# Kernel optimization log

Hardware: AMD Instinct MI355X
Metric: run time of the kernel (lower is better)

## Reference

```python
import jax, jax.numpy as jnp
import numpy as np

EPS = 1e-8


def _lstm_cell(xx, h, c, Wih, Whh, bih, bhh):
    g = xx @ Wih.T + bih + h @ Whh.T + bhh
    i, f, gg, o = jnp.split(g, 4, axis=-1)
    i = jax.nn.sigmoid(i); f = jax.nn.sigmoid(f); o = jax.nn.sigmoid(o)
    c2 = f * c + i * jnp.tanh(gg)
    return o * jnp.tanh(c2), c2


def _layernorm(t):
    mu = t.mean(-1, keepdims=True)
    var = t.var(-1, keepdims=True)
    return (t - mu) / jnp.sqrt(var + 1e-5)


def _dnc_forward(x, memory0, Wy, WE, Wr, lstm_params):
    bs, T, xd = x.shape
    N, W = memory0.shape[1], memory0.shape[2]
    R = Wr.shape[0] // W
    hdim = lstm_params[0][1].shape[2]
    L = len(lstm_params)

    def step(carry, x_t):
        M, lrw, u, lww, lrv, h, c = carry
        # BatchNorm1d (training-mode batch stats, affine=identity)
        bn = (x_t - x_t.mean(0)) / jnp.sqrt(x_t.var(0) + 1e-5)
        layer_in = jnp.concatenate([bn, lrv.reshape(bs, W * R)], axis=1)
        # bidirectional multi-layer LSTM, single timestep
        hs, cs = [], []
        for l in range(L):
            Wih, Whh, bih, bhh = lstm_params[l]
            hf, cf = _lstm_cell(layer_in, h[2 * l], c[2 * l], Wih[0], Whh[0], bih[0], bhh[0])
            hb, cb = _lstm_cell(layer_in, h[2 * l + 1], c[2 * l + 1], Wih[1], Whh[1], bih[1], bhh[1])
            layer_in = jnp.concatenate([hf, hb], axis=1)
            hs += [hf, hb]; cs += [cf, cb]
        h_new = jnp.stack(hs); c_new = jnp.stack(cs)  # (2L, bs, h)
        flat = jnp.transpose(h_new, (1, 0, 2)).reshape(bs, 2 * L * hdim)
        vt = flat @ Wy
        iv = _layernorm(flat @ WE)
        # interface parsing (E_t = W*R + 3W + 3R + 3)
        i0 = W * R
        rkeys = iv[:, :i0].reshape(bs, W, R)
        rbeta = 1.0 - jax.nn.log_sigmoid(iv[:, i0:i0 + R]); i0 += R
        wkey = iv[:, i0:i0 + W]; i0 += W
        wbeta = 1.0 - jax.nn.log_sigmoid(iv[:, i0:i0 + 1]); i0 += 1
        erase = jax.nn.sigmoid(iv[:, i0:i0 + W]); i0 += W
        wvec = iv[:, i0:i0 + W]; i0 += W
        fgates = jax.nn.sigmoid(iv[:, i0:i0 + R]); i0 += R
        ag = jax.nn.sigmoid(iv[:, i0:i0 + 1]); i0 += 1
        wg = jax.nn.sigmoid(iv[:, i0:i0 + 1]); i0 += 1
        # read_modes: softmax over a singleton dim -> all ones (content-only read)
        # memory retention and usage
        retention = jnp.prod(1.0 - fgates[:, None, :] * lrw, axis=2)  # (bs, N)
        u_new = (u + lww - u * lww) * retention
        # allocation weighting (sort ascending usage, exclusive cumprod)
        idx = jnp.argsort(u_new, axis=1)
        su = jnp.take_along_axis(u_new, idx, axis=1)
        cp = jnp.cumprod(su, axis=1)
        cp = jnp.concatenate([jnp.ones((bs, 1), su.dtype), cp[:, :-1]], axis=1)
        a_sorted = (1.0 - su) * cp
        alloc = jnp.take_along_axis(a_sorted, jnp.argsort(idx, axis=1), axis=1)
        # write weighting: content + allocation
        Mn = M / (jnp.linalg.norm(M, axis=2, keepdims=True) + EPS)
        kn = wkey / (jnp.linalg.norm(wkey, axis=1, keepdims=True) + EPS)
        cw = jax.nn.softmax(wbeta * jnp.einsum('bnw,bw->bn', Mn, kn), axis=1)
        ww = wg * (ag * alloc + (1.0 - ag) * cw)  # (bs, N)
        # write to memory
        M_new = M * (1.0 - ww[:, :, None] * erase[:, None, :]) + ww[:, :, None] * wvec[:, None, :]
        # content read weightings against updated memory
        Mn2 = M_new / (jnp.linalg.norm(M_new, axis=2, keepdims=True) + EPS)
        rkn = rkeys / (jnp.linalg.norm(rkeys, axis=1, keepdims=True) + EPS)
        sim = jnp.einsum('bnw,bwr->bnr', Mn2, rkn)
        rw = jax.nn.softmax(rbeta[:, None, :] * sim, axis=1)  # (bs, N, R)
        rv = jnp.einsum('bnw,bnr->bwr', M_new, rw)            # (bs, W, R)
        yt = vt + rv.reshape(bs, W * R) @ Wr
        return (M_new, rw, u_new, ww, rv, h_new, c_new), yt

    z = lambda *s: jnp.zeros(s, x.dtype)
    init = (memory0, z(bs, N, R), z(bs, N), z(bs, N), z(bs, W, R),
            z(2 * L, bs, hdim), z(2 * L, bs, hdim))
    _, yts = jax.lax.scan(step, init, jnp.transpose(x, (1, 0, 2)))
    return jnp.max(yts, axis=0)  # max over timesteps, (bs, v_t)


def setup_inputs() -> dict:
    key = jax.random.key(0)
    ks = jax.random.split(key, 16)
    bs, T, xd = 32, 32, 128
    hdim, L, v_t, W, R, N = 512, 2, 2048, 64, 4, 1024
    E_t = W * R + 3 * W + 3 * R + 3  # 463
    u = lambda k, shape, s: jax.random.uniform(k, shape, jnp.float32, -s, s)
    in0, in1 = xd + R * W, 2 * hdim
    sh = 1.0 / np.sqrt(hdim)
    inp = {
        'x': jax.random.normal(ks[0], (bs, T, xd), jnp.float32),
        'memory0': u(ks[1], (bs, N, W), 1.0 / np.sqrt(W)),
        'Wy': u(ks[2], (2 * L * hdim, v_t), 1.0 / np.sqrt(v_t)),
        'WE': u(ks[3], (2 * L * hdim, E_t), 1.0 / np.sqrt(E_t)),
        'Wr': u(ks[4], (W * R, v_t), 1.0 / np.sqrt(v_t)),
        'Wih0': u(ks[5], (2, 4 * hdim, in0), sh),
        'Whh0': u(ks[6], (2, 4 * hdim, hdim), sh),
        'bih0': u(ks[7], (2, 4 * hdim), sh),
        'bhh0': u(ks[8], (2, 4 * hdim), sh),
        'Wih1': u(ks[9], (2, 4 * hdim, in1), sh),
        'Whh1': u(ks[10], (2, 4 * hdim, hdim), sh),
        'bih1': u(ks[11], (2, 4 * hdim), sh),
        'bhh1': u(ks[12], (2, 4 * hdim), sh),
    }
    return inp


def reference(x, memory0, Wy, WE, Wr, Wih0, Whh0, bih0, bhh0, Wih1, Whh1, bih1, bhh1):
    lstm_params = [(Wih0, Whh0, bih0, bhh0), (Wih1, Whh1, bih1, bhh1)]
    return _dnc_forward(x, memory0, Wy, WE, Wr, lstm_params)
```

## Files before the change

### kernel.cpp

```cpp
#include <hip/hip_runtime.h>
#include <math.h>

#define BSZ 32
#define TT  32
#define XD  128
#define HD  512
#define VT  2048
#define ET  463
#define GKS 8
#define VKS 16

__device__ __forceinline__ float sigf(float x){ return 1.f/(1.f+expf(-x)); }
__device__ __forceinline__ float logsigf(float x){
    return (x >= 0.f) ? -log1pf(expf(-x)) : x - log1pf(expf(x));
}

__device__ __forceinline__ float bsum(float v, float* red, int tid){
    #pragma unroll
    for (int off = 32; off > 0; off >>= 1) v += __shfl_xor(v, off);
    if ((tid & 63) == 0) red[tid >> 6] = v;
    __syncthreads();
    if (tid == 0){
        float s = red[0];
        #pragma unroll
        for (int i = 1; i < 16; ++i) s += red[i];
        red[16] = s;
    }
    __syncthreads();
    float r = red[16];
    __syncthreads();
    return r;
}
__device__ __forceinline__ float bmax(float v, float* red, int tid){
    #pragma unroll
    for (int off = 32; off > 0; off >>= 1) v = fmaxf(v, __shfl_xor(v, off));
    if ((tid & 63) == 0) red[tid >> 6] = v;
    __syncthreads();
    if (tid == 0){
        float s = red[0];
        #pragma unroll
        for (int i = 1; i < 16; ++i) s = fmaxf(s, red[i]);
        red[16] = s;
    }
    __syncthreads();
    float r = red[16];
    __syncthreads();
    return r;
}

__global__ void dnc_bnx(const float* __restrict__ x, float* __restrict__ bnx){
    int t = blockIdx.x, k = threadIdx.x;
    float vals[BSZ];
    float s = 0.f;
    #pragma unroll
    for (int b = 0; b < BSZ; ++b){ vals[b] = x[(b*TT + t)*XD + k]; s += vals[b]; }
    float mean = s * (1.f/BSZ);
    float ss = 0.f;
    #pragma unroll
    for (int b = 0; b < BSZ; ++b){ float d = vals[b]-mean; ss += d*d; }
    float inv = 1.f / sqrtf(ss*(1.f/BSZ) + 1e-5f);
    #pragma unroll
    for (int b = 0; b < BSZ; ++b) bnx[((size_t)t*BSZ + b)*XD + k] = (vals[b]-mean)*inv;
}

__device__ __forceinline__ void lstm_gemm_body(
    const float* __restrict__ srcA, int KA,
    const float* __restrict__ srcB, int KB,
    const float* __restrict__ hbase,
    const float* __restrict__ Wih, const float* __restrict__ Whh,
    float* __restrict__ gpart, int jc, int d, int ks, int tid,
    float* itile, float* wtile)
{
    const int jg = tid & 31, bg = tid >> 5;
    const int jbase = jc*128;
    const int j0 = jbase + jg*4;
    const int jg4 = jg*4;
    const int b0 = bg*4;
    const int K1 = KA + KB;
    const int cA = KA >> 6;
    const int cin = K1 >> 6;
    const int nct = cin + 8;
    const int per = (nct + GKS - 1) / GKS;
    int c0 = ks*per; int c1 = min(nct, c0+per);
    float acc[4][4] = {{0}};
    for (int c = c0; c < c1; ++c){
        const float* src; int stride, kb, wcol; const float* Wb; int Kw;
        if (c < cA){ src = srcA; stride = KA; kb = c*64; wcol = c*64;
                     Wb = Wih + (size_t)d*2048*K1; Kw = K1; }
        else if (c < cin){ src = srcB; stride = KB; kb = (c-cA)*64; wcol = c*64;
                           Wb = Wih + (size_t)d*2048*K1; Kw = K1; }
        else { src = hbase + d*(BSZ*HD); stride = HD; kb = (c-cin)*64; wcol = kb;
               Wb = Whh + (size_t)d*2048*512; Kw = 512; }
        #pragma unroll
        for (int i = 0; i < 8; ++i){
            int idx = i*256 + tid; int kk = idx & 63, b = idx >> 6;
            itile[kk*36 + b] = src[b*stride + kb + kk];
        }
        #pragma unroll
        for (int i = 0; i < 8; ++i){
            int fi = i*256 + tid;
            int j  = fi & 127;
            int kq = fi >> 7;
            float4 w4 = *(const float4*)&Wb[(size_t)(jbase + j)*Kw + wcol + kq*4];
            wtile[(kq*4+0)*132 + j] = w4.x;
            wtile[(kq*4+1)*132 + j] = w4.y;
            wtile[(kq*4+2)*132 + j] = w4.z;
            wtile[(kq*4+3)*132 + j] = w4.w;
        }
        __syncthreads();
        #pragma unroll 8
        for (int kk = 0; kk < 64; ++kk){
            float4 a = *(const float4*)&itile[kk*36 + b0];
            float4 w = *(const float4*)&wtile[kk*132 + jg4];
            acc[0][0] += w.x*a.x; acc[0][1] += w.x*a.y; acc[0][2] += w.x*a.z; acc[0][3] += w.x*a.w;
            acc[1][0] += w.y*a.x; acc[1][1] += w.y*a.y; acc[1][2] += w.y*a.z; acc[1][3] += w.y*a.w;
            acc[2][0] += w.z*a.x; acc[2][1] += w.z*a.y; acc[2][2] += w.z*a.z; acc[2][3] += w.z*a.w;
            acc[3][0] += w.w*a.x; acc[3][1] += w.w*a.y; acc[3][2] += w.w*a.z; acc[3][3] += w.w*a.w;
        }
        __syncthreads();
    }
    #pragma unroll
    for (int jj = 0; jj < 4; ++jj){
        #pragma unroll
        for (int bb = 0; bb < 4; ++bb)
            gpart[((size_t)(d*GKS + ks)*BSZ + (b0+bb))*2048 + (j0+jj)] = acc[jj][bb];
    }
}

__device__ __forceinline__ void yfin_body(
    const float* __restrict__ lrv, const float* __restrict__ Wr,
    const float* __restrict__ vtp, float* __restrict__ out, int t,
    int mi, int bgi, int tid, float* lt)
{
    const int mg = tid & 31, bgl = tid >> 5;
    const int m0 = mi*128 + mg*4;
    const int b  = bgi*8 + bgl;
    #pragma unroll
    for (int i = 0; i < 8; ++i)
        lt[tid*9 + i] = lrv[((size_t)(bgi*8 + i))*256 + tid];
    __syncthreads();
    float4 acc = make_float4(0.f,0.f,0.f,0.f);
    for (int kk = 0; kk < 256; ++kk){
        float av = lt[kk*9 + bgl];
        float4 wv = *(const float4*)&Wr[(size_t)kk*VT + m0];
        acc.x += av*wv.x; acc.y += av*wv.y; acc.z += av*wv.z; acc.w += av*wv.w;
    }
    #pragma unroll
    for (int sp = 0; sp < VKS; ++sp){
        float4 vp = *(const float4*)&vtp[((size_t)sp*BSZ + b)*VT + m0];
        acc.x += vp.x; acc.y += vp.y; acc.z += vp.z; acc.w += vp.w;
    }
    float4* op = (float4*)&out[(size_t)b*VT + m0];
    if (t == 0){ *op = acc; }
    else {
        float4 cur = *op;
        cur.x = fmaxf(cur.x, acc.x); cur.y = fmaxf(cur.y, acc.y);
        cur.z = fmaxf(cur.z, acc.z); cur.w = fmaxf(cur.w, acc.w);
        *op = cur;
    }
}

__global__ __launch_bounds__(256) void dnc_gemm0_yfin(
    const float* __restrict__ srcA,
    const float* __restrict__ lrv, const float* __restrict__ hbase,
    const float* __restrict__ Wih, const float* __restrict__ Whh,
    float* __restrict__ gpart,
    const float* __restrict__ Wr, const float* __restrict__ vtp,
    float* __restrict__ out, int tprev)
{
    __shared__ __align__(16) float itile[64*36];
    __shared__ __align__(16) float wtile[64*132];
    const int bid = blockIdx.x, tid = threadIdx.x;
    if (bid < 256){
        lstm_gemm_body(srcA, XD, lrv, 256, hbase, Wih, Whh, gpart,
                       bid & 15, (bid >> 4) & 1, bid >> 5, tid, itile, wtile);
    } else {
        if (tprev < 0) return;
        int yb = bid - 256;
        yfin_body(lrv, Wr, vtp, out, tprev, yb & 15, yb >> 4, tid, itile);
    }
}

__global__ __launch_bounds__(256) void dnc_lstm_gemm(
    const float* __restrict__ srcA, int KA,
    const float* __restrict__ srcB, int KB,
    const float* __restrict__ hbase,
    const float* __restrict__ Wih, const float* __restrict__ Whh,
    float* __restrict__ gpart)
{
    __shared__ __align__(16) float itile[64*36];
    __shared__ __align__(16) float wtile[64*132];
    lstm_gemm_body(srcA, KA, srcB, KB, hbase, Wih, Whh, gpart,
                   blockIdx.x, blockIdx.y, blockIdx.z, threadIdx.x, itile, wtile);
}

__global__ void dnc_yfin(const float* __restrict__ lrv, const float* __restrict__ Wr,
                         const float* __restrict__ vtp, float* __restrict__ out, int t){
    __shared__ float lt[256*9];
    yfin_body(lrv, Wr, vtp, out, t, blockIdx.x, blockIdx.y, threadIdx.x, lt);
}

__global__ void dnc_gates(const float* __restrict__ gpart,
                          const float* __restrict__ bih, const float* __restrict__ bhh,
                          float* __restrict__ cstate, float* __restrict__ hwrite,
                          float* __restrict__ flat, float* __restrict__ lout, int l){
    int idx = blockIdx.x*256 + threadIdx.x;
    int u = idx & 511, b = (idx >> 9) & 31, d = idx >> 14;
    int cell = 2*l + d;
    float g[4];
    #pragma unroll
    for (int xg = 0; xg < 4; ++xg){
        int j = xg*512 + u;
        float s = bih[d*2048 + j] + bhh[d*2048 + j];
        #pragma unroll
        for (int ks = 0; ks < GKS; ++ks)
            s += gpart[((size_t)(d*GKS + ks)*BSZ + b)*2048 + j];
        g[xg] = s;
    }
    float ig = sigf(g[0]), fg = sigf(g[1]), og = sigf(g[3]);
    float gg = tanhf(g[2]);
    int ci = (cell*BSZ + b)*HD + u;
    float c2 = fg*cstate[ci] + ig*gg;
    cstate[ci] = c2;
    float h = og*tanhf(c2);
    hwrite[ci] = h;
    flat[b*2048 + cell*HD + u] = h;
    if (lout) lout[b*1024 + d*HD + u] = h;
}

__global__ void dnc_gemv2(const float* __restrict__ fin, const float* __restrict__ Wy,
                          const float* __restrict__ WE,
                          float* __restrict__ vtp, float* __restrict__ ep){
    const int bx = blockIdx.x, ksi = blockIdx.y;
    const int tid = threadIdx.x;
    const int lane = tid & 63, bg = tid >> 6;
    const int b0 = bg*8;
    const int k0 = ksi*128;
    __shared__ __align__(16) float tile[128*36];
    #pragma unroll
    for (int i = 0; i < 16; ++i){
        int idx = i*256 + tid; int kk = idx & 127, b = idx >> 7;
        tile[kk*36 + b] = fin[b*2048 + k0 + kk];
    }
    __syncthreads();

    if (bx < 8){
        const int m = bx*256 + lane*4;
        float acc[8][4] = {{0}};
        #pragma unroll 4
        for (int kk = 0; kk < 128; ++kk){
            float4 w  = *(const float4*)&Wy[(size_t)(k0+kk)*VT + m];
            float4 a0 = *(const float4*)&tile[kk*36 + b0];
            float4 a1 = *(const float4*)&tile[kk*36 + b0 + 4];
            acc[0][0]+=a0.x*w.x; acc[0][1]+=a0.x*w.y; acc[0][2]+=a0.x*w.z; acc[0][3]+=a0.x*w.w;
            acc[1][0]+=a0.y*w.x; acc[1][1]+=a0.y*w.y; acc[1][2]+=a0.y*w.z; acc[1][3]+=a0.y*w.w;
            acc[2][0]+=a0.z*w.x; acc[2][1]+=a0.z*w.y; acc[2][2]+=a0.z*w.z; acc[2][3]+=a0.z*w.w;
            acc[3][0]+=a0.w*w.x; acc[3][1]+=a0.w*w.y; acc[3][2]+=a0.w*w.z; acc[3][3]+=a0.w*w.w;
            acc[4][0]+=a1.x*w.x; acc[4][1]+=a1.x*w.y; acc[4][2]+=a1.x*w.z; acc[4][3]+=a1.x*w.w;
            acc[5][0]+=a1.y*w.x; acc[5][1]+=a1.y*w.y; acc[5][2]+=a1.y*w.z; acc[5][3]+=a1.y*w.w;
            acc[6][0]+=a1.z*w.x; acc[6][1]+=a1.z*w.y; acc[6][2]+=a1.z*w.z; acc[6][3]+=a1.z*w.w;
            acc[7][0]+=a1.w*w.x; acc[7][1]+=a1.w*w.y; acc[7][2]+=a1.w*w.z; acc[7][3]+=a1.w*w.w;
        }
        #pragma unroll
        for (int bb = 0; bb < 8; ++bb){
            float4 st = make_float4(acc[bb][0], acc[bb][1], acc[bb][2], acc[bb][3]);
            *(float4*)&vtp[((size_t)ksi*BSZ + b0+bb)*VT + m] = st;
        }
    } else {
        const int mb = bx - 8;
        const int m0 = mb*128 + lane, m1 = m0 + 64;
        bool v0 = m0 < ET, v1 = m1 < ET;
        float acc[16] = {0};
        #pragma unroll 2
        for (int kk = 0; kk < 128; ++kk){
            float4 pq = *(const float4*)&tile[kk*36 + b0];
            float4 qq = *(const float4*)&tile[kk*36 + b0 + 4];
            const float* wr = WE + (size_t)(k0+kk)*ET;
            float w0 = v0 ? wr[m0] : 0.f;
            float w1 = v1 ? wr[m1] : 0.f;
            acc[0]+=pq.x*w0; acc[1]+=pq.y*w0; acc[2]+=pq.z*w0; acc[3]+=pq.w*w0;
            acc[4]+=qq.x*w0; acc[5]+=qq.y*w0; acc[6]+=qq.z*w0; acc[7]+=qq.w*w0;
            acc[8]+=pq.x*w1; acc[9]+=pq.y*w1; acc[10]+=pq.z*w1; acc[11]+=pq.w*w1;
            acc[12]+=qq.x*w1; acc[13]+=qq.y*w1; acc[14]+=qq.z*w1; acc[15]+=qq.w*w1;
        }
        if (v0){
            #pragma unroll
            for (int bb = 0; bb < 8; ++bb)
                ep[((size_t)ksi*BSZ + b0+bb)*ET + m0] = acc[bb];
        }
        if (v1){
            #pragma unroll
            for (int bb = 0; bb < 8; ++bb)
                ep[((size_t)ksi*BSZ + b0+bb)*ET + m1] = acc[8+bb];
        }
    }
}

__global__ __launch_bounds__(1024) void dnc_presort_cw(
    const float* __restrict__ ep, const float* __restrict__ lrw,
    const float* __restrict__ lww, float* __restrict__ ubuf,
    float* __restrict__ iv, float* __restrict__ allocw,
    const float* __restrict__ M, float* __restrict__ scw)
{
    const int bid = blockIdx.x, tid = threadIdx.x;
    const int lane = tid & 63, wid = tid >> 6;
    __shared__ float red[32];
    __shared__ float ivS[464];
    __shared__ unsigned long long keysS[1024];
    __shared__ float wtot[16], wpref[16];

    if (bid < 32){
        const int b = bid;
        float myv = 0.f;
        if (tid < ET){
            #pragma unroll
            for (int s = 0; s < VKS; ++s) myv += ep[((size_t)s*BSZ + b)*ET + tid];
        }
        float mean = bsum(myv, red, tid) * (1.f/ET);
        float dd = (tid < ET) ? (myv - mean) : 0.f;
        float var = bsum(dd*dd, red, tid) * (1.f/ET);
        float rinv = 1.f / sqrtf(var + 1e-5f);
        float ivv = (myv - mean)*rinv;
        if (tid < ET){ ivS[tid] = ivv; iv[b*ET + tid] = ivv; }
        __syncthreads();

        const int n = tid;
        float4 lw4 = *(const float4*)&lrw[((size_t)b*1024 + n)*4];
        float f0 = sigf(ivS[453]), f1 = sigf(ivS[454]), f2 = sigf(ivS[455]), f3 = sigf(ivS[456]);
        float ret = (1.f-f0*lw4.x)*(1.f-f1*lw4.y)*(1.f-f2*lw4.z)*(1.f-f3*lw4.w);
        float uo = ubuf[b*1024+n], lwo = lww[b*1024+n];
        float un = (uo + lwo - uo*lwo)*ret;
        ubuf[b*1024+n] = un;

        unsigned long long key = ((unsigned long long)__float_as_uint(un) << 32) | (unsigned)tid;
        for (int k = 2; k <= 1024; k <<= 1){
            int j = k >> 1;
            for (; j >= 64; j >>= 1){
                keysS[tid] = key; __syncthreads();
                unsigned long long other = keysS[tid ^ j];
                bool up = ((tid & k) == 0);
                bool takeMin = (((tid & j) == 0) == up);
                key = takeMin ? (key < other ? key : other) : (key > other ? key : other);
                __syncthreads();
            }
            for (; j >= 1; j >>= 1){
                unsigned long long other = __shfl_xor(key, j);
                bool up = ((tid & k) == 0);
                bool takeMin = (((tid & j) == 0) == up);
                key = takeMin ? (key < other ? key : other) : (key > other ? key : other);
            }
        }
        float su = __uint_as_float((unsigned)(key >> 32));
        int idxv = (int)(key & 0xffffffffu);

        float p = su;
        #pragma unroll
        for (int o = 1; o < 64; o <<= 1){ float q = __shfl_up(p, o); if (lane >= o) p *= q; }
        if (lane == 63) wtot[wid] = p;
        __syncthreads();
        if (tid == 0){
            float r = 1.f;
            #pragma unroll
            for (int i = 0; i < 16; ++i){ wpref[i] = r; r *= wtot[i]; }
        }
        __syncthreads();
        float excl = __shfl_up(p, 1); if (lane == 0) excl = 1.f;
        float cpx = excl * wpref[wid];
        allocw[b*1024 + idxv] = (1.f - su)*cpx;
    } else {
        const int b = bid - 32;
        float myv = 0.f;
        if (tid < ET){
            #pragma unroll
            for (int s = 0; s < VKS; ++s) myv += ep[((size_t)s*BSZ + b)*ET + tid];
        }
        float mean = bsum(myv, red, tid) * (1.f/ET);
        float dd = (tid < ET) ? (myv - mean) : 0.f;
        float var = bsum(dd*dd, red, tid) * (1.f/ET);
        float rinv = 1.f / sqrtf(var + 1e-5f);
        float ivv = (myv - mean)*rinv;
        if (tid >= 260 && tid < 324) ivS[tid - 260] = ivv;
        if (tid == 324) ivS[64] = 1.f - logsigf(ivv);
        __syncthreads();
        float ksq = 0.f;
        #pragma unroll
        for (int w = 0; w < 64; ++w) ksq += ivS[w]*ivS[w];
        float kden = sqrtf(ksq) + 1e-8f;
        float wb = ivS[64];
        const float* Mrow = M + ((size_t)b*1024 + tid)*64;
        float dot = 0.f, msq = 0.f;
        #pragma unroll
        for (int w = 0; w < 64; w += 4){
            float4 mv = *(const float4*)(Mrow + w);
            dot += mv.x*ivS[w] + mv.y*ivS[w+1] + mv.z*ivS[w+2] + mv.w*ivS[w+3];
            msq += mv.x*mv.x + mv.y*mv.y + mv.z*mv.z + mv.w*mv.w;
        }
        scw[b*1024 + tid] = wb*dot/((sqrtf(msq) + 1e-8f)*kden);
    }
}

__global__ __launch_bounds__(1024) void dnc_memup_rv(
    float* __restrict__ M, const float* __restrict__ scw,
    const float* __restrict__ allocw, const float* __restrict__ iv,
    float* __restrict__ lww, float* __restrict__ lrw, float* __restrict__ lrv)
{
    const int b = blockIdx.x, tid = threadIdx.x;
    const int lane = tid & 63, wid = tid >> 6;
    __shared__ float red[32];
    __shared__ float aux[400];
    __shared__ float pS[4096];
    __shared__ float rvS[4096];
    const int n = tid;

    float s = scw[b*1024 + n];
    float mx = bmax(s, red, tid);
    float tot = bsum(expf(s - mx), red, tid);
    float cwv = expf(s - mx)/tot;
    float ag = sigf(iv[b*ET + 457]), wg = sigf(iv[b*ET + 458]);
    float wwv = wg*(ag*allocw[b*1024 + n] + (1.f-ag)*cwv);
    lww[b*1024 + n] = wwv;

    if (tid < 64){ aux[tid] = sigf(iv[b*ET + 325 + tid]); aux[64+tid] = iv[b*ET + 389 + tid]; }
    if (tid >= 64 && tid < 320) aux[64 + tid] = iv[b*ET + (tid - 64)];
    if (tid >= 320 && tid < 324) aux[72 + tid] = 1.f - logsigf(iv[b*ET + 256 + (tid - 320)]);
    __syncthreads();
    if (tid < 4){
        float ss = 0.f;
        #pragma unroll
        for (int w = 0; w < 64; ++w){ float v = aux[128 + w*4 + tid]; ss += v*v; }
        aux[384 + tid] = sqrtf(ss) + 1e-8f;
    }
    __syncthreads();
    if (tid < 256) aux[128 + tid] = aux[128 + tid] / aux[384 + (tid & 3)];
    __syncthreads();

    float* Mrow = M + ((size_t)b*1024 + n)*64;
    float dr0=0.f, dr1=0.f, dr2=0.f, dr3=0.f, msq2=0.f;
    #pragma unroll
    for (int w = 0; w < 64; w += 4){
        float4 mv = *(const float4*)(Mrow + w);
        mv.x = mv.x*(1.f - wwv*aux[w+0]) + wwv*aux[64+w+0];
        mv.y = mv.y*(1.f - wwv*aux[w+1]) + wwv*aux[64+w+1];
        mv.z = mv.z*(1.f - wwv*aux[w+2]) + wwv*aux[64+w+2];
        mv.w = mv.w*(1.f - wwv*aux[w+3]) + wwv*aux[64+w+3];
        *(float4*)(Mrow + w) = mv;
        msq2 += mv.x*mv.x + mv.y*mv.y + mv.z*mv.z + mv.w*mv.w;
        dr0 += mv.x*aux[128+(w+0)*4+0] + mv.y*aux[128+(w+1)*4+0] + mv.z*aux[128+(w+2)*4+0] + mv.w*aux[128+(w+3)*4+0];
        dr1 += mv.x*aux[128+(w+0)*4+1] + mv.y*aux[128+(w+1)*4+1] + mv.z*aux[128+(w+2)*4+1] + mv.w*aux[128+(w+3)*4+1];
        dr2 += mv.x*aux[128+(w+0)*4+2] + mv.y*aux[128+(w+1)*4+2] + mv.z*aux[128+(w+2)*4+2] + mv.w*aux[128+(w+3)*4+2];
        dr3 += mv.x*aux[128+(w+0)*4+3] + mv.y*aux[128+(w+1)*4+3] + mv.z*aux[128+(w+2)*4+3] + mv.w*aux[128+(w+3)*4+3];
    }
    float den = sqrtf(msq2) + 1e-8f;
    pS[0*1024 + n] = aux[392]*dr0/den;
    pS[1*1024 + n] = aux[393]*dr1/den;
    pS[2*1024 + n] = aux[394]*dr2/den;
    pS[3*1024 + n] = aux[395]*dr3/den;
    __syncthreads();

    const int r_ = tid >> 8, i4 = (tid & 255)*4;
    float v0 = pS[r_*1024 + i4+0], v1 = pS[r_*1024 + i4+1];
    float v2 = pS[r_*1024 + i4+2], v3 = pS[r_*1024 + i4+3];
    float lm = fmaxf(fmaxf(v0,v1), fmaxf(v2,v3));
    #pragma unroll
    for (int off = 32; off > 0; off >>= 1) lm = fmaxf(lm, __shfl_xor(lm, off));
    if (lane == 0) red[wid] = lm;
    __syncthreads();
    if (tid < 4) red[16+tid] = fmaxf(fmaxf(red[4*tid],red[4*tid+1]), fmaxf(red[4*tid+2],red[4*tid+3]));
    __syncthreads();
    float mxr = red[16 + r_];
    float lsum = expf(v0-mxr) + expf(v1-mxr) + expf(v2-mxr) + expf(v3-mxr);
    #pragma unroll
    for (int off = 32; off > 0; off >>= 1) lsum += __shfl_xor(lsum, off);
    if (lane == 0) red[wid] = lsum;
    __syncthreads();
    if (tid < 4) red[20+tid] = red[4*tid]+red[4*tid+1]+red[4*tid+2]+red[4*tid+3];
    __syncthreads();
    float totr = red[20 + r_];
    {
        lrw[((size_t)(b*1024 + i4+0))*4 + r_] = expf(v0-mxr)/totr;
        lrw[((size_t)(b*1024 + i4+1))*4 + r_] = expf(v1-mxr)/totr;
        lrw[((size_t)(b*1024 + i4+2))*4 + r_] = expf(v2-mxr)/totr;
        lrw[((size_t)(b*1024 + i4+3))*4 + r_] = expf(v3-mxr)/totr;
    }
    __syncthreads();

    {
        const int w = tid & 63, g = tid >> 6;
        const float* Mb = M + (size_t)b*65536;
        const float* rwb = lrw + (size_t)b*4096;
        float a0=0.f, a1=0.f, a2=0.f, a3=0.f;
        #pragma unroll 4
        for (int i = 0; i < 64; ++i){
            int n2 = g*64 + i;
            float m = Mb[(size_t)n2*64 + w];
            float4 rw4 = *(const float4*)&rwb[n2*4];
            a0 += m*rw4.x; a1 += m*rw4.y; a2 += m*rw4.z; a3 += m*rw4.w;
        }
        rvS[(0*16 + g)*64 + w] = a0;
        rvS[(1*16 + g)*64 + w] = a1;
        rvS[(2*16 + g)*64 + w] = a2;
        rvS[(3*16 + g)*64 + w] = a3;
    }
    __syncthreads();
    if (tid < 256){
        int w2 = tid >> 2, r2 = tid & 3;
        float ssum = 0.f;
        #pragma unroll
        for (int g = 0; g < 16; ++g) ssum += rvS[(r2*16 + g)*64 + w2];
        lrv[b*256 + tid] = ssum;
    }
}

extern "C" void kernel_launch(void* const* d_in, const int* in_sizes, int n_in,
                              void* d_out, int out_size, void* d_ws, size_t ws_size,
                              hipStream_t stream){
    const float* x      = (const float*)d_in[0];
    const float* mem0   = (const float*)d_in[1];
    const float* Wy     = (const float*)d_in[2];
    const float* WE     = (const float*)d_in[3];
    const float* Wr     = (const float*)d_in[4];
    const float* Wih0   = (const float*)d_in[5];
    const float* Whh0   = (const float*)d_in[6];
    const float* bih0   = (const float*)d_in[7];
    const float* bhh0   = (const float*)d_in[8];
    const float* Wih1   = (const float*)d_in[9];
    const float* Whh1   = (const float*)d_in[10];
    const float* bih1   = (const float*)d_in[11];
    const float* bhh1   = (const float*)d_in[12];
    float* out = (float*)d_out;

    float* p = (float*)d_ws;
    float* M       = p; p += (size_t)BSZ*1024*64;
    float* hstate0 = p; p += 4*BSZ*HD;
    float* hstate1 = p; p += 4*BSZ*HD;
    float* cstate  = p; p += 4*BSZ*HD;
    float* ubuf    = p; p += BSZ*1024;
    float* lww     = p; p += BSZ*1024;
    float* lrw     = p; p += BSZ*1024*4;
    float* lrv     = p; p += BSZ*256;
    float* bnx     = p; p += (size_t)TT*BSZ*XD;
    float* lin1    = p; p += BSZ*1024;
    float* gpart   = p; p += (size_t)2*GKS*BSZ*2048;
    float* flat    = p; p += BSZ*2048;
    float* vtp     = p; p += (size_t)VKS*BSZ*VT;
    float* ep      = p; p += (size_t)VKS*BSZ*ET;
    float* iv      = p; p += BSZ*ET;
    float* allocw  = p; p += BSZ*1024;
    float* scw     = p; p += BSZ*1024;

    (void)hipMemcpyAsync(M, mem0, (size_t)BSZ*1024*64*sizeof(float), hipMemcpyDeviceToDevice, stream);
    size_t zfloats = (size_t)(4*BSZ*HD)*3 + BSZ*1024*2 + BSZ*1024*4 + BSZ*256;
    (void)hipMemsetAsync(hstate0, 0, zfloats*sizeof(float), stream);

    dnc_bnx<<<TT, 128, 0, stream>>>(x, bnx);

    for (int t = 0; t < TT; ++t){
        const float* hr = (t & 1) ? hstate1 : hstate0;
        float*       hw = (t & 1) ? hstate0 : hstate1;
        dnc_gemm0_yfin<<<320, 256, 0, stream>>>(bnx + (size_t)t*BSZ*XD,
            lrv, hr, Wih0, Whh0, gpart, Wr, vtp, out, t - 1);
        dnc_gates<<<128, 256, 0, stream>>>(gpart, bih0, bhh0, cstate, hw, flat, lin1, 0);
        dnc_lstm_gemm<<<dim3(16,2,GKS), 256, 0, stream>>>(lin1, 1024,
            nullptr, 0, hr + 2*BSZ*HD, Wih1, Whh1, gpart);
        dnc_gates<<<128, 256, 0, stream>>>(gpart, bih1, bhh1, cstate, hw, flat, nullptr, 1);
        dnc_gemv2<<<dim3(12,VKS), 256, 0, stream>>>(flat, Wy, WE, vtp, ep);
        dnc_presort_cw<<<64, 1024, 0, stream>>>(ep, lrw, lww, ubuf, iv, allocw, M, scw);
        dnc_memup_rv<<<32, 1024, 0, stream>>>(M, scw, allocw, iv, lww, lrw, lrv);
    }
    dnc_yfin<<<dim3(16,4), 256, 0, stream>>>(lrv, Wr, vtp, out, TT - 1);
}
```

Measured before the change: 3.919 ms.

## Move Wy GEMV into presort kernel and prefetch weights in registers

The fused output/interface GEMV is split. The WE (interface) part stays as its own small kernel on the critical path. The Wy (output vector) part is moved into extra blocks of the presort/content-weight kernel, so it overlaps with the memory-addressing work instead of delaying it. Both GEMV loops now software-prefetch the next 8 weight rows into registers. The cost is higher register pressure and a larger presort launch, whose 1024-thread Wy blocks use more shared memory.

Result: slower. 8.823 ms (+125.1%).

```diff
diff --git a/kernel.cpp b/kernel.cpp
--- a/kernel.cpp
+++ b/kernel.cpp
@@ -228,13 +228,13 @@
     if (lout) lout[b*1024 + d*HD + u] = h;
 }
 
-__global__ void dnc_gemv2(const float* __restrict__ fin, const float* __restrict__ Wy,
-                          const float* __restrict__ WE,
-                          float* __restrict__ vtp, float* __restrict__ ep){
-    const int bx = blockIdx.x, ksi = blockIdx.y;
+__global__ void dnc_gemv_we(const float* __restrict__ fin, const float* __restrict__ WE,
+                            float* __restrict__ ep){
+    const int mb = blockIdx.x, ksi = blockIdx.y;
     const int tid = threadIdx.x;
     const int lane = tid & 63, bg = tid >> 6;
     const int b0 = bg*8;
+    const int m0 = mb*128 + lane, m1 = m0 + 64;
     const int k0 = ksi*128;
     __shared__ __align__(16) float tile[128*36];
     #pragma unroll
@@ -243,56 +243,43 @@
         tile[kk*36 + b] = fin[b*2048 + k0 + kk];
     }
     __syncthreads();
-
-    if (bx < 8){
-        const int m = bx*256 + lane*4;
-        float acc[8][4] = {{0}};
-        #pragma unroll 4
-        for (int kk = 0; kk < 128; ++kk){
-            float4 w  = *(const float4*)&Wy[(size_t)(k0+kk)*VT + m];
-            float4 a0 = *(const float4*)&tile[kk*36 + b0];
-            float4 a1 = *(const float4*)&tile[kk*36 + b0 + 4];
-            acc[0][0]+=a0.x*w.x; acc[0][1]+=a0.x*w.y; acc[0][2]+=a0.x*w.z; acc[0][3]+=a0.x*w.w;
-            acc[1][0]+=a0.y*w.x; acc[1][1]+=a0.y*w.y; acc[1][2]+=a0.y*w.z; acc[1][3]+=a0.y*w.w;
-            acc[2][0]+=a0.z*w.x; acc[2][1]+=a0.z*w.y; acc[2][2]+=a0.z*w.z; acc[2][3]+=a0.z*w.w;
-            acc[3][0]+=a0.w*w.x; acc[3][1]+=a0.w*w.y; acc[3][2]+=a0.w*w.z; acc[3][3]+=a0.w*w.w;
-            acc[4][0]+=a1.x*w.x; acc[4][1]+=a1.x*w.y; acc[4][2]+=a1.x*w.z; acc[4][3]+=a1.x*w.w;
-            acc[5][0]+=a1.y*w.x; acc[5][1]+=a1.y*w.y; acc[5][2]+=a1.y*w.z; acc[5][3]+=a1.y*w.w;
-            acc[6][0]+=a1.z*w.x; acc[6][1]+=a1.z*w.y; acc[6][2]+=a1.z*w.z; acc[6][3]+=a1.z*w.w;
-            acc[7][0]+=a1.w*w.x; acc[7][1]+=a1.w*w.y; acc[7][2]+=a1.w*w.z; acc[7][3]+=a1.w*w.w;
-        }
-        #pragma unroll
-        for (int bb = 0; bb < 8; ++bb){
-            float4 st = make_float4(acc[bb][0], acc[bb][1], acc[bb][2], acc[bb][3]);
-            *(float4*)&vtp[((size_t)ksi*BSZ + b0+bb)*VT + m] = st;
-        }
-    } else {
-        const int mb = bx - 8;
-        const int m0 = mb*128 + lane, m1 = m0 + 64;
-        bool v0 = m0 < ET, v1 = m1 < ET;
-        float acc[16] = {0};
-        #pragma unroll 2
-        for (int kk = 0; kk < 128; ++kk){
+    bool v0 = m0 < ET, v1 = m1 < ET;
+    float w0r[8], w1r[8];
+    #pragma unroll
+    for (int i = 0; i < 8; ++i){
+        const float* wr = WE + (size_t)(k0+i)*ET;
+        w0r[i] = v0 ? wr[m0] : 0.f;
+        w1r[i] = v1 ? wr[m1] : 0.f;
+    }
+    float acc[16] = {0};
+    for (int kb = 0; kb < 128; kb += 8){
+        #pragma unroll
+        for (int i = 0; i < 8; ++i){
+            int kk = kb + i;
+            float w0 = w0r[i], w1 = w1r[i];
+            int kn = kk + 8;
+            if (kn < 128){
+                const float* wr = WE + (size_t)(k0+kn)*ET;
+                w0r[i] = v0 ? wr[m0] : 0.f;
+                w1r[i] = v1 ? wr[m1] : 0.f;
+            }
             float4 pq = *(const float4*)&tile[kk*36 + b0];
             float4 qq = *(const float4*)&tile[kk*36 + b0 + 4];
-            const float* wr = WE + (size_t)(k0+kk)*ET;
-            float w0 = v0 ? wr[m0] : 0.f;
-            float w1 = v1 ? wr[m1] : 0.f;
             acc[0]+=pq.x*w0; acc[1]+=pq.y*w0; acc[2]+=pq.z*w0; acc[3]+=pq.w*w0;
             acc[4]+=qq.x*w0; acc[5]+=qq.y*w0; acc[6]+=qq.z*w0; acc[7]+=qq.w*w0;
             acc[8]+=pq.x*w1; acc[9]+=pq.y*w1; acc[10]+=pq.z*w1; acc[11]+=pq.w*w1;
             acc[12]+=qq.x*w1; acc[13]+=qq.y*w1; acc[14]+=qq.z*w1; acc[15]+=qq.w*w1;
         }
-        if (v0){
-            #pragma unroll
-            for (int bb = 0; bb < 8; ++bb)
-                ep[((size_t)ksi*BSZ + b0+bb)*ET + m0] = acc[bb];
-        }
-        if (v1){
-            #pragma unroll
-            for (int bb = 0; bb < 8; ++bb)
-                ep[((size_t)ksi*BSZ + b0+bb)*ET + m1] = acc[8+bb];
-        }
+    }
+    if (v0){
+        #pragma unroll
+        for (int bb = 0; bb < 8; ++bb)
+            ep[((size_t)ksi*BSZ + b0+bb)*ET + m0] = acc[bb];
+    }
+    if (v1){
+        #pragma unroll
+        for (int bb = 0; bb < 8; ++bb)
+            ep[((size_t)ksi*BSZ + b0+bb)*ET + m1] = acc[8+bb];
     }
 }
 
@@ -300,7 +287,9 @@
     const float* __restrict__ ep, const float* __restrict__ lrw,
     const float* __restrict__ lww, float* __restrict__ ubuf,
     float* __restrict__ iv, float* __restrict__ allocw,
-    const float* __restrict__ M, float* __restrict__ scw)
+    const float* __restrict__ M, float* __restrict__ scw,
+    const float* __restrict__ fin, const float* __restrict__ Wy,
+    float* __restrict__ vtp)
 {
     const int bid = blockIdx.x, tid = threadIdx.x;
     const int lane = tid & 63, wid = tid >> 6;
@@ -308,6 +297,7 @@
     __shared__ float ivS[464];
     __shared__ unsigned long long keysS[1024];
     __shared__ float wtot[16], wpref[16];
+    __shared__ __align__(16) float tile[128*36];
 
     if (bid < 32){
         const int b = bid;
@@ -367,7 +357,7 @@
         float excl = __shfl_up(p, 1); if (lane == 0) excl = 1.f;
         float cpx = excl * wpref[wid];
         allocw[b*1024 + idxv] = (1.f - su)*cpx;
-    } else {
+    } else if (bid < 64){
         const int b = bid - 32;
         float myv = 0.f;
         if (tid < ET){
@@ -396,6 +386,48 @@
             msq += mv.x*mv.x + mv.y*mv.y + mv.z*mv.z + mv.w*mv.w;
         }
         scw[b*1024 + tid] = wb*dot/((sqrtf(msq) + 1e-8f)*kden);
+    } else {
+        const int yb = bid - 64;
+        const int ksi = yb >> 1, half = yb & 1;
+        const int k0 = ksi*128;
+        #pragma unroll
+        for (int i = 0; i < 4; ++i){
+            int idx = i*1024 + tid; int kk = idx & 127, b = idx >> 7;
+            tile[kk*36 + b] = fin[b*2048 + k0 + kk];
+        }
+        __syncthreads();
+        const int sub = tid >> 8, stid = tid & 255;
+        const int slane = stid & 63, sbg = stid >> 6;
+        const int b0 = sbg*8;
+        const int m = (half*4 + sub)*256 + slane*4;
+        float4 wreg[8];
+        #pragma unroll
+        for (int i = 0; i < 8; ++i) wreg[i] = *(const float4*)&Wy[(size_t)(k0+i)*VT + m];
+        float acc[8][4] = {{0}};
+        for (int kb = 0; kb < 128; kb += 8){
+            #pragma unroll
+            for (int i = 0; i < 8; ++i){
+                const int kk = kb + i;
+                float4 w = wreg[i];
+                int kn = kk + 8;
+                if (kn < 128) wreg[i] = *(const float4*)&Wy[(size_t)(k0+kn)*VT + m];
+                float4 a0 = *(const float4*)&tile[kk*36 + b0];
+                float4 a1 = *(const float4*)&tile[kk*36 + b0 + 4];
+                acc[0][0]+=a0.x*w.x; acc[0][1]+=a0.x*w.y; acc[0][2]+=a0.x*w.z; acc[0][3]+=a0.x*w.w;
+                acc[1][0]+=a0.y*w.x; acc[1][1]+=a0.y*w.y; acc[1][2]+=a0.y*w.z; acc[1][3]+=a0.y*w.w;
+                acc[2][0]+=a0.z*w.x; acc[2][1]+=a0.z*w.y; acc[2][2]+=a0.z*w.z; acc[2][3]+=a0.z*w.w;
+                acc[3][0]+=a0.w*w.x; acc[3][1]+=a0.w*w.y; acc[3][2]+=a0.w*w.z; acc[3][3]+=a0.w*w.w;
+                acc[4][0]+=a1.x*w.x; acc[4][1]+=a1.x*w.y; acc[4][2]+=a1.x*w.z; acc[4][3]+=a1.x*w.w;
+                acc[5][0]+=a1.y*w.x; acc[5][1]+=a1.y*w.y; acc[5][2]+=a1.y*w.z; acc[5][3]+=a1.y*w.w;
+                acc[6][0]+=a1.z*w.x; acc[6][1]+=a1.z*w.y; acc[6][2]+=a1.z*w.z; acc[6][3]+=a1.z*w.w;
+                acc[7][0]+=a1.w*w.x; acc[7][1]+=a1.w*w.y; acc[7][2]+=a1.w*w.z; acc[7][3]+=a1.w*w.w;
+            }
+        }
+        #pragma unroll
+        for (int bb = 0; bb < 8; ++bb){
+            float4 st = make_float4(acc[bb][0], acc[bb][1], acc[bb][2], acc[bb][3]);
+            *(float4*)&vtp[((size_t)ksi*BSZ + b0+bb)*VT + m] = st;
+        }
     }
 }
 
@@ -563,8 +595,9 @@
         dnc_lstm_gemm<<<dim3(16,2,GKS), 256, 0, stream>>>(lin1, 1024,
             nullptr, 0, hr + 2*BSZ*HD, Wih1, Whh1, gpart);
         dnc_gates<<<128, 256, 0, stream>>>(gpart, bih1, bhh1, cstate, hw, flat, nullptr, 1);
-        dnc_gemv2<<<dim3(12,VKS), 256, 0, stream>>>(flat, Wy, WE, vtp, ep);
-        dnc_presort_cw<<<64, 1024, 0, stream>>>(ep, lrw, lww, ubuf, iv, allocw, M, scw);
+        dnc_gemv_we<<<dim3(4,16), 256, 0, stream>>>(flat, WE, ep);
+        dnc_presort_cw<<<96, 1024, 0, stream>>>(ep, lrw, lww, ubuf, iv, allocw, M, scw,
+                                                flat, Wy, vtp);
         dnc_memup_rv<<<32, 1024, 0, stream>>>(M, scw, allocw, iv, lww, lrw, lrv);
     }
     dnc_yfin<<<dim3(16,4), 256, 0, stream>>>(lrv, Wr, vtp, out, TT - 1);
```

## Split vt/interface GEMV K across more blocks and register-prefetch weight rows

Applied to the files above, without the earlier changes.

Doubles the K-split count for the Wy/WE output projection (VKS 16 to 32), halving each block's K range to 64 so twice as many blocks stream the weights in parallel. Adds an 8-deep register ring that prefetches weight rows ahead of use, so global loads overlap the FMAs. The cost is twice as many partial sums for the downstream reduction to read and add, plus extra register pressure from the prefetch buffers.

Result: slower. 6.955 ms (+77.4%).

```diff
diff --git a/kernel.cpp b/kernel.cpp
--- a/kernel.cpp
+++ b/kernel.cpp
@@ -8,7 +8,7 @@
 #define VT  2048
 #define ET  463
 #define GKS 8
-#define VKS 16
+#define VKS 32
 
 __device__ __forceinline__ float sigf(float x){ return 1.f/(1.f+expf(-x)); }
 __device__ __forceinline__ float logsigf(float x){
@@ -235,31 +235,39 @@
     const int tid = threadIdx.x;
     const int lane = tid & 63, bg = tid >> 6;
     const int b0 = bg*8;
-    const int k0 = ksi*128;
-    __shared__ __align__(16) float tile[128*36];
-    #pragma unroll
-    for (int i = 0; i < 16; ++i){
-        int idx = i*256 + tid; int kk = idx & 127, b = idx >> 7;
+    const int k0 = ksi*64;
+    __shared__ __align__(16) float tile[64*36];
+    #pragma unroll
+    for (int i = 0; i < 8; ++i){
+        int idx = i*256 + tid; int kk = idx & 63, b = idx >> 6;
         tile[kk*36 + b] = fin[b*2048 + k0 + kk];
     }
     __syncthreads();
 
     if (bx < 8){
         const int m = bx*256 + lane*4;
+        float4 wreg[8];
+        #pragma unroll
+        for (int i = 0; i < 8; ++i) wreg[i] = *(const float4*)&Wy[(size_t)(k0+i)*VT + m];
         float acc[8][4] = {{0}};
-        #pragma unroll 4
-        for (int kk = 0; kk < 128; ++kk){
-            float4 w  = *(const float4*)&Wy[(size_t)(k0+kk)*VT + m];
-            float4 a0 = *(const float4*)&tile[kk*36 + b0];
-            float4 a1 = *(const float4*)&tile[kk*36 + b0 + 4];
-            acc[0][0]+=a0.x*w.x; acc[0][1]+=a0.x*w.y; acc[0][2]+=a0.x*w.z; acc[0][3]+=a0.x*w.w;
-            acc[1][0]+=a0.y*w.x; acc[1][1]+=a0.y*w.y; acc[1][2]+=a0.y*w.z; acc[1][3]+=a0.y*w.w;
-            acc[2][0]+=a0.z*w.x; acc[2][1]+=a0.z*w.y; acc[2][2]+=a0.z*w.z; acc[2][3]+=a0.z*w.w;
-            acc[3][0]+=a0.w*w.x; acc[3][1]+=a0.w*w.y; acc[3][2]+=a0.w*w.z; acc[3][3]+=a0.w*w.w;
-            acc[4][0]+=a1.x*w.x; acc[4][1]+=a1.x*w.y; acc[4][2]+=a1.x*w.z; acc[4][3]+=a1.x*w.w;
-            acc[5][0]+=a1.y*w.x; acc[5][1]+=a1.y*w.y; acc[5][2]+=a1.y*w.z; acc[5][3]+=a1.y*w.w;
-            acc[6][0]+=a1.z*w.x; acc[6][1]+=a1.z*w.y; acc[6][2]+=a1.z*w.z; acc[6][3]+=a1.z*w.w;
-            acc[7][0]+=a1.w*w.x; acc[7][1]+=a1.w*w.y; acc[7][2]+=a1.w*w.z; acc[7][3]+=a1.w*w.w;
+        for (int kb = 0; kb < 64; kb += 8){
+            #pragma unroll
+            for (int i = 0; i < 8; ++i){
+                const int kk = kb + i;
+                float4 w = wreg[i];
+                int kn = kk + 8;
+                if (kn < 64) wreg[i] = *(const float4*)&Wy[(size_t)(k0+kn)*VT + m];
+                float4 a0 = *(const float4*)&tile[kk*36 + b0];
+                float4 a1 = *(const float4*)&tile[kk*36 + b0 + 4];
+                acc[0][0]+=a0.x*w.x; acc[0][1]+=a0.x*w.y; acc[0][2]+=a0.x*w.z; acc[0][3]+=a0.x*w.w;
+                acc[1][0]+=a0.y*w.x; acc[1][1]+=a0.y*w.y; acc[1][2]+=a0.y*w.z; acc[1][3]+=a0.y*w.w;
+                acc[2][0]+=a0.z*w.x; acc[2][1]+=a0.z*w.y; acc[2][2]+=a0.z*w.z; acc[2][3]+=a0.z*w.w;
+                acc[3][0]+=a0.w*w.x; acc[3][1]+=a0.w*w.y; acc[3][2]+=a0.w*w.z; acc[3][3]+=a0.w*w.w;
+                acc[4][0]+=a1.x*w.x; acc[4][1]+=a1.x*w.y; acc[4][2]+=a1.x*w.z; acc[4][3]+=a1.x*w.w;
+                acc[5][0]+=a1.y*w.x; acc[5][1]+=a1.y*w.y; acc[5][2]+=a1.y*w.z; acc[5][3]+=a1.y*w.w;
+                acc[6][0]+=a1.z*w.x; acc[6][1]+=a1.z*w.y; acc[6][2]+=a1.z*w.z; acc[6][3]+=a1.z*w.w;
+                acc[7][0]+=a1.w*w.x; acc[7][1]+=a1.w*w.y; acc[7][2]+=a1.w*w.z; acc[7][3]+=a1.w*w.w;
+            }
         }
         #pragma unroll
         for (int bb = 0; bb < 8; ++bb){
@@ -270,18 +278,32 @@
         const int mb = bx - 8;
         const int m0 = mb*128 + lane, m1 = m0 + 64;
         bool v0 = m0 < ET, v1 = m1 < ET;
+        float w0r[8], w1r[8];
+        #pragma unroll
+        for (int i = 0; i < 8; ++i){
+            const float* wr = WE + (size_t)(k0+i)*ET;
+            w0r[i] = v0 ? wr[m0] : 0.f;
+            w1r[i] = v1 ? wr[m1] : 0.f;
+        }
         float acc[16] = {0};
-        #pragma unroll 2
-        for (int kk = 0; kk < 128; ++kk){
-            float4 pq = *(const float4*)&tile[kk*36 + b0];
-            float4 qq = *(const float4*)&tile[kk*36 + b0 + 4];
-            const float* wr = WE + (size_t)(k0+kk)*ET;
-            float w0 = v0 ? wr[m0] : 0.f;
-            float w1 = v1 ? wr[m1] : 0.f;
-            acc[0]+=pq.x*w0; acc[1]+=pq.y*w0; acc[2]+=pq.z*w0; acc[3]+=pq.w*w0;
-            acc[4]+=qq.x*w0; acc[5]+=qq.y*w0; acc[6]+=qq.z*w0; acc[7]+=qq.w*w0;
-            acc[8]+=pq.x*w1; acc[9]+=pq.y*w1; acc[10]+=pq.z*w1; acc[11]+=pq.w*w1;
-            acc[12]+=qq.x*w1; acc[13]+=qq.y*w1; acc[14]+=qq.z*w1; acc[15]+=qq.w*w1;
+        for (int kb = 0; kb < 64; kb += 8){
+            #pragma unroll
+            for (int i = 0; i < 8; ++i){
+                int kk = kb + i;
+                float w0 = w0r[i], w1 = w1r[i];
+                int kn = kk + 8;
+                if (kn < 64){
+                    const float* wr = WE + (size_t)(k0+kn)*ET;
+                    w0r[i] = v0 ? wr[m0] : 0.f;
+                    w1r[i] = v1 ? wr[m1] : 0.f;
+                }
+                float4 pq = *(const float4*)&tile[kk*36 + b0];
+                float4 qq = *(const float4*)&tile[kk*36 + b0 + 4];
+                acc[0]+=pq.x*w0; acc[1]+=pq.y*w0; acc[2]+=pq.z*w0; acc[3]+=pq.w*w0;
+                acc[4]+=qq.x*w0; acc[5]+=qq.y*w0; acc[6]+=qq.z*w0; acc[7]+=qq.w*w0;
+                acc[8]+=pq.x*w1; acc[9]+=pq.y*w1; acc[10]+=pq.z*w1; acc[11]+=pq.w*w1;
+                acc[12]+=qq.x*w1; acc[13]+=qq.y*w1; acc[14]+=qq.z*w1; acc[15]+=qq.w*w1;
+            }
         }
         if (v0){
             #pragma unroll
```
